# Kernel optimization log

Hardware: AMD Instinct MI355X
Metric: run time of the kernel (lower is better)

## Reference

```python
import jax, jax.numpy as jnp
import numpy as np

E = 16      # num_experts
K = 4       # num_experts_per_tok
H = 2048    # hidden_size
I = 1408    # moe_intermediate_size
SI = 5632   # shared expert intermediate size
CAP = 1024
NORM_TOPK = False


def setup_inputs() -> dict:
    key = jax.random.key(0)
    ks = jax.random.split(key, 9)
    def w(k, shape, fan_in):
        return jax.random.normal(k, shape, jnp.float32) * (fan_in ** -0.5)
    return {
        "hidden_states": jax.random.normal(ks[0], (1, 2048, H), jnp.float32),
        "gate_w":  w(ks[1], (E, H), H),        # router: Linear(H -> E), no bias
        "we_gate": w(ks[2], (E, I, H), H),     # per-expert gate_proj weights
        "we_up":   w(ks[3], (E, I, H), H),     # per-expert up_proj weights
        "we_down": w(ks[4], (E, H, I), I),     # per-expert down_proj weights
        "ws_gate": w(ks[5], (SI, H), H),       # shared expert gate_proj
        "ws_up":   w(ks[6], (SI, H), H),       # shared expert up_proj
        "ws_down": w(ks[7], (H, SI), SI),      # shared expert down_proj
        "sg_w":    w(ks[8], (1, H), H),        # shared_expert_gate: Linear(H -> 1)
    }


def reference(hidden_states, gate_w, we_gate, we_up, we_down,
              ws_gate, ws_up, ws_down, sg_w):
    B, S, Hd = hidden_states.shape
    x = hidden_states.reshape(-1, Hd)                      # [T, H]
    T = x.shape[0]

    # --- router ---
    router_logits = x @ gate_w.T                           # [T, E]
    probs = jax.nn.softmax(router_logits.astype(jnp.float32), axis=-1)
    topw, topi = jax.lax.top_k(probs, K)                   # [T, K]
    if NORM_TOPK:
        topw = topw / topw.sum(axis=-1, keepdims=True)

    # --- dispatch: flatten (token, slot) assignments ---
    A = T * K
    fe = topi.reshape(A)                                   # expert id per assignment
    fw = topw.reshape(A)                                   # routing weight per assignment
    ft = jnp.repeat(jnp.arange(T), K)                      # token id per assignment
    # position of each assignment within its expert (rank in arrival order)
    oh = jax.nn.one_hot(fe, E, dtype=jnp.int32)            # [A, E]
    pos = jnp.take_along_axis(jnp.cumsum(oh, axis=0) - 1, fe[:, None], axis=1)[:, 0]
    valid = pos < CAP
    # scatter tokens into per-expert buffers; overflow goes to dummy row CAP
    buf = jnp.zeros((E, CAP + 1, Hd), x.dtype)
    buf = buf.at[fe, jnp.where(valid, pos, CAP)].set(x[ft])[:, :CAP]  # [E, C, H]

    # --- per-expert SiLU-gated MLP (batched grouped GEMMs) ---
    g = jnp.einsum('ech,eih->eci', buf, we_gate)
    u = jnp.einsum('ech,eih->eci', buf, we_up)
    eo = jnp.einsum('eci,ehi->ech', jax.nn.silu(g) * u, we_down)      # [E, C, H]

    # --- combine: weighted scatter-add back to tokens ---
    ga = eo[fe, jnp.minimum(pos, CAP - 1)]                 # [A, H]
    wcomb = (fw * valid.astype(fw.dtype)).astype(x.dtype)
    y = jnp.zeros((T, Hd), x.dtype).at[ft].add(ga * wcomb[:, None])

    # --- shared expert with sigmoid gate ---
    sh = (jax.nn.silu(x @ ws_gate.T) * (x @ ws_up.T)) @ ws_down.T
    sh = jax.nn.sigmoid(x @ sg_w.T) * sh

    out = (y + sh).reshape(B, S, Hd)
    return out, router_logits
```

## Files before the change

### kernel.cpp

```cpp
#include <hip/hip_runtime.h>

#define T_TOK 2048
#define NE 16
#define KTOP 4
#define HD 2048
#define ID 1408
#define SID 5632
#define CAPACITY 1024

typedef __attribute__((ext_vector_type(8))) short short8;
typedef __attribute__((ext_vector_type(4))) float floatx4;

__device__ __forceinline__ short f2b(float f){
  union { float f; unsigned u; } v; v.f = f;
  unsigned r = v.u + 0x7fffu + ((v.u >> 16) & 1u);
  return (short)(r >> 16);
}
__device__ __forceinline__ float b2f(short s){
  union { float f; unsigned u; } v; v.u = ((unsigned)(unsigned short)s) << 16;
  return v.f;
}
__device__ __forceinline__ unsigned cvt_pk(float a, float b){
  unsigned r;
  asm("v_cvt_pk_bf16_f32 %0, %1, %2" : "=v"(r) : "v"(a), "v"(b));
  return r;
}
__device__ __forceinline__ short8 cvt8(float4 a, float4 b){
  union { unsigned d[4]; short8 s; } u;
  u.d[0] = cvt_pk(a.x, a.y); u.d[1] = cvt_pk(a.z, a.w);
  u.d[2] = cvt_pk(b.x, b.y); u.d[3] = cvt_pk(b.z, b.w);
  return u.s;
}
__device__ __forceinline__ void gl16(const void* g, void* l){
  __builtin_amdgcn_global_load_lds(
      (const __attribute__((address_space(1))) void*)g,
      (__attribute__((address_space(3))) void*)l, 16, 0, 0);
}

__global__ void moe_zero(int* __restrict__ counts){
  if (threadIdx.x < NE) counts[threadIdx.x] = 0;
}

__global__ void moe_router(const float* __restrict__ x,
                           const float* __restrict__ gate_w,
                           const float* __restrict__ sg_w,
                           float* __restrict__ logits_out,
                           short* __restrict__ xb,
                           int* __restrict__ counts,
                           int* __restrict__ slot_token,
                           float* __restrict__ slot_w,
                           int* __restrict__ tslot,
                           float* __restrict__ tw,
                           float* __restrict__ sg)
{
  int wave = threadIdx.x >> 6, lane = threadIdx.x & 63;
  int t = (blockIdx.x << 2) + wave;
  if (t >= T_TOK) return;
  const float4* xr = (const float4*)(x + (size_t)t * HD);
  short8* xbw = (short8*)(xb + (size_t)t * HD);
  float acc[17];
  #pragma unroll
  for (int e = 0; e < 17; ++e) acc[e] = 0.f;
  #pragma unroll
  for (int j = 0; j < 4; ++j){
    int i4 = (j * 64 + lane) * 2;
    float4 x0 = xr[i4], x1 = xr[i4 + 1];
    xbw[j * 64 + lane] = cvt8(x0, x1);
    #pragma unroll
    for (int e = 0; e < 16; ++e){
      const float4* gr = (const float4*)(gate_w + e * HD);
      float4 g0 = gr[i4], g1 = gr[i4 + 1];
      acc[e] += x0.x*g0.x + x0.y*g0.y + x0.z*g0.z + x0.w*g0.w
              + x1.x*g1.x + x1.y*g1.y + x1.z*g1.z + x1.w*g1.w;
    }
    const float4* sr = (const float4*)sg_w;
    float4 s0 = sr[i4], s1 = sr[i4 + 1];
    acc[16] += x0.x*s0.x + x0.y*s0.y + x0.z*s0.z + x0.w*s0.w
             + x1.x*s1.x + x1.y*s1.y + x1.z*s1.z + x1.w*s1.w;
  }
  #pragma unroll
  for (int e = 0; e < 17; ++e){
    float v = acc[e];
    #pragma unroll
    for (int off = 32; off > 0; off >>= 1) v += __shfl_xor(v, off, 64);
    acc[e] = v;
  }
  if (lane == 0){
    float m = acc[0];
    #pragma unroll
    for (int e = 1; e < 16; ++e) m = fmaxf(m, acc[e]);
    float p[16]; float s = 0.f;
    #pragma unroll
    for (int e = 0; e < 16; ++e){ p[e] = expf(acc[e] - m); s += p[e]; }
    float inv = 1.f / s;
    #pragma unroll
    for (int e = 0; e < 16; ++e) logits_out[t * 16 + e] = acc[e];
    unsigned used = 0;
    for (int k = 0; k < KTOP; ++k){
      float best = -1.f; int bi = 0;
      #pragma unroll
      for (int e = 0; e < 16; ++e){
        float pe = ((used >> e) & 1u) ? -1.f : p[e];
        if (pe > best){ best = pe; bi = e; }
      }
      used |= (1u << bi);
      int pos = atomicAdd(&counts[bi], 1);
      int enc = -1;
      if (pos < CAPACITY){
        slot_token[bi * CAPACITY + pos] = t;
        slot_w[bi * CAPACITY + pos] = best * inv;
        enc = bi * CAPACITY + pos;
      }
      tslot[t * KTOP + k] = enc;
      tw[t * KTOP + k] = best * inv;
    }
    sg[t] = 1.f / (1.f + expf(-acc[16]));
  }
}


__global__ __launch_bounds__(256) void moe_gateup(
    const short* __restrict__ Asrc,
    const float* __restrict__ Wg_, const float* __restrict__ Wu_,
    short* __restrict__ Out,
    const int* __restrict__ counts, const int* __restrict__ slot_token,
    int Ndim, int Kdim, int expert_mode, int mtiles, int ntiles)
{
  int nwg = gridDim.x;
  int wg = ((blockIdx.x & 7) * (nwg >> 3)) + (blockIdx.x >> 3);
  int m_t = wg % mtiles; wg /= mtiles;
  int n_t = wg % ntiles; int e = wg / ntiles;

  int cnt = T_TOK; size_t woff = 0; short* out = Out;
  if (expert_mode){
    cnt = counts[e]; if (cnt > CAPACITY) cnt = CAPACITY;
    if (m_t * 128 >= cnt) return;
    woff = (size_t)e * Ndim * Kdim;
    out = Out + (size_t)e * CAPACITY * Ndim;
  }
  const int m0 = m_t * 128, n0 = n_t * 64;

  __shared__ __align__(16) char smem[2][32768];

  const int tid = threadIdx.x;
  const int lane = tid & 63, wave = tid >> 6;
  const int wr = wave >> 1, wc = wave & 1;
  const int lrow = lane & 15, lk = lane >> 4;

  const int srow = tid >> 3, pslot = tid & 7;
  const int lslot = pslot ^ (srow & 7);

  const short* aptr[4];
  #pragma unroll
  for (int i = 0; i < 4; ++i){
    int p = m0 + i * 32 + srow;
    const short* base;
    if (expert_mode){
      int q = (p < cnt) ? p : 0;
      base = Asrc + (size_t)slot_token[e * CAPACITY + q] * Kdim;
    } else base = Asrc + (size_t)p * Kdim;
    aptr[i] = base + (lslot << 3);
  }
  const float *bsrc[4];
  #pragma unroll
  for (int i = 0; i < 2; ++i){
    size_t roff = (size_t)(n0 + i * 32 + srow) * Kdim + (lslot << 3);
    bsrc[i]     = Wg_ + woff + roff;
    bsrc[i + 2] = Wu_ + woff + roff;
  }

  const floatx4 vzero = {0.f, 0.f, 0.f, 0.f};
  floatx4 accg[4][2], accu[4][2];
  #pragma unroll
  for (int i = 0; i < 4; ++i)
    #pragma unroll
    for (int j = 0; j < 2; ++j){ accg[i][j] = vzero; accu[i][j] = vzero; }

  const int fxor = lrow & 7;
  const int arowb = (wr * 64 + lrow) << 7;
  const int browb = (wc * 32 + lrow) << 7;
  const int bwoff = 16384 + (tid << 4);

  float4 breg[4][2];
  #pragma unroll
  for (int i = 0; i < 4; ++i) gl16(aptr[i], smem[0] + i * 4096 + tid * 16);
  #pragma unroll
  for (int i = 0; i < 4; ++i){
    breg[i][0] = *(const float4*)(bsrc[i]);
    breg[i][1] = *(const float4*)(bsrc[i] + 4);
  }
  #pragma unroll
  for (int i = 0; i < 4; ++i)
    *(short8*)(smem[0] + bwoff + i * 4096) = cvt8(breg[i][0], breg[i][1]);
  __syncthreads();

  int cur = 0;
  for (int k0 = 0; k0 < Kdim; k0 += 64){
    const bool more = (k0 + 64) < Kdim;
    if (more){
      #pragma unroll
      for (int i = 0; i < 4; ++i) gl16(aptr[i] + k0 + 64, smem[cur ^ 1] + i * 4096 + tid * 16);
      #pragma unroll
      for (int i = 0; i < 4; ++i){
        breg[i][0] = *(const float4*)(bsrc[i] + k0 + 64);
        breg[i][1] = *(const float4*)(bsrc[i] + k0 + 68);
      }
    }
    const char* bb = smem[cur];
    #pragma unroll
    for (int kh = 0; kh < 2; ++kh){
      const int soff = (((kh << 2) | lk) ^ fxor) << 4;
      short8 a[4], bg[2], bu[2];
      #pragma unroll
      for (int mf = 0; mf < 4; ++mf)
        a[mf] = *(const short8*)(bb + arowb + (mf << 11) + soff);
      #pragma unroll
      for (int nf = 0; nf < 2; ++nf){
        bg[nf] = *(const short8*)(bb + 16384 + browb + (nf << 11) + soff);
        bu[nf] = *(const short8*)(bb + 24576 + browb + (nf << 11) + soff);
      }
      #pragma unroll
      for (int mf = 0; mf < 4; ++mf)
        #pragma unroll
        for (int nf = 0; nf < 2; ++nf){
          accg[mf][nf] = __builtin_amdgcn_mfma_f32_16x16x32_bf16(a[mf], bg[nf], accg[mf][nf], 0, 0, 0);
          accu[mf][nf] = __builtin_amdgcn_mfma_f32_16x16x32_bf16(a[mf], bu[nf], accu[mf][nf], 0, 0, 0);
        }
    }
    if (more){
      #pragma unroll
      for (int i = 0; i < 4; ++i)
        *(short8*)(smem[cur ^ 1] + bwoff + i * 4096) = cvt8(breg[i][0], breg[i][1]);
    }
    __syncthreads();
    cur ^= 1;
  }

  const int colbase = n0 + wc * 32 + lrow;
  #pragma unroll
  for (int mf = 0; mf < 4; ++mf){
    int pr = m0 + wr * 64 + mf * 16 + lk * 4;
    #pragma unroll
    for (int nf = 0; nf < 2; ++nf){
      floatx4 g4 = accg[mf][nf], u4 = accu[mf][nf];
      int col = colbase + nf * 16;
      #pragma unroll
      for (int r = 0; r < 4; ++r){
        float gv = g4[r], uv = u4[r];
        float a = (gv / (1.f + __expf(-gv))) * uv;
        out[(size_t)(pr + r) * Ndim + col] = f2b(a);
      }
    }
  }
}

template<int NF>
__global__ __launch_bounds__(256) void moe_down(
    const short* __restrict__ Asrc, const float* __restrict__ Wd_,
    float* __restrict__ y, short* __restrict__ eo,
    const int* __restrict__ counts, const int* __restrict__ slot_token,
    const float* __restrict__ slot_w, const float* __restrict__ sgate,
    int Kdim, int expert_mode, int mtiles, int ntiles)
{
  constexpr int BN = NF * 32;
  int nwg = gridDim.x;
  int wg = ((blockIdx.x & 7) * (nwg >> 3)) + (blockIdx.x >> 3);
  int m_t = wg % mtiles; wg /= mtiles;
  int n_t = wg % ntiles; int e = wg / ntiles;

  int cnt = T_TOK; const short* ab = Asrc; size_t woff = 0;
  if (expert_mode){
    cnt = counts[e]; if (cnt > CAPACITY) cnt = CAPACITY;
    if (m_t * 128 >= cnt) return;
    ab = Asrc + (size_t)e * CAPACITY * Kdim;
    woff = (size_t)e * HD * Kdim;
  }
  const int m0 = m_t * 128, n0 = n_t * BN;

  __shared__ __align__(16) char smem[2][16384 + NF * 4096];

  const int tid = threadIdx.x;
  const int lane = tid & 63, wave = tid >> 6;
  const int wr = wave >> 1, wc = wave & 1;
  const int lrow = lane & 15, lk = lane >> 4;

  const int srow = tid >> 3, pslot = tid & 7;
  const int lslot = pslot ^ (srow & 7);

  const short* aptr[4];
  #pragma unroll
  for (int i = 0; i < 4; ++i)
    aptr[i] = ab + (size_t)(m0 + i * 32 + srow) * Kdim + (lslot << 3);
  const float* bsrc[NF];
  #pragma unroll
  for (int i = 0; i < NF; ++i)
    bsrc[i] = Wd_ + woff + (size_t)(n0 + i * 32 + srow) * Kdim + (lslot << 3);

  const floatx4 vzero = {0.f, 0.f, 0.f, 0.f};
  floatx4 acc[4][NF];
  #pragma unroll
  for (int i = 0; i < 4; ++i)
    #pragma unroll
    for (int j = 0; j < NF; ++j) acc[i][j] = vzero;

  const int fxor = lrow & 7;
  const int arowb = (wr * 64 + lrow) << 7;
  const int browb = (wc * (NF * 16) + lrow) << 7;
  const int bwoff = 16384 + (tid << 4);

  float4 breg[NF][2];
  #pragma unroll
  for (int i = 0; i < 4; ++i) gl16(aptr[i], smem[0] + i * 4096 + tid * 16);
  #pragma unroll
  for (int i = 0; i < NF; ++i){
    breg[i][0] = *(const float4*)(bsrc[i]);
    breg[i][1] = *(const float4*)(bsrc[i] + 4);
  }
  #pragma unroll
  for (int i = 0; i < NF; ++i)
    *(short8*)(smem[0] + bwoff + i * 4096) = cvt8(breg[i][0], breg[i][1]);
  __syncthreads();

  int cur = 0;
  for (int k0 = 0; k0 < Kdim; k0 += 64){
    const bool more = (k0 + 64) < Kdim;
    if (more){
      #pragma unroll
      for (int i = 0; i < 4; ++i) gl16(aptr[i] + k0 + 64, smem[cur ^ 1] + i * 4096 + tid * 16);
      #pragma unroll
      for (int i = 0; i < NF; ++i){
        breg[i][0] = *(const float4*)(bsrc[i] + k0 + 64);
        breg[i][1] = *(const float4*)(bsrc[i] + k0 + 68);
      }
    }
    const char* bb = smem[cur];
    #pragma unroll
    for (int kh = 0; kh < 2; ++kh){
      const int soff = (((kh << 2) | lk) ^ fxor) << 4;
      short8 a[4], b[NF];
      #pragma unroll
      for (int mf = 0; mf < 4; ++mf)
        a[mf] = *(const short8*)(bb + arowb + (mf << 11) + soff);
      #pragma unroll
      for (int nf = 0; nf < NF; ++nf)
        b[nf] = *(const short8*)(bb + 16384 + browb + (nf << 11) + soff);
      #pragma unroll
      for (int mf = 0; mf < 4; ++mf)
        #pragma unroll
        for (int nf = 0; nf < NF; ++nf)
          acc[mf][nf] = __builtin_amdgcn_mfma_f32_16x16x32_bf16(a[mf], b[nf], acc[mf][nf], 0, 0, 0);
    }
    if (more){
      #pragma unroll
      for (int i = 0; i < NF; ++i)
        *(short8*)(smem[cur ^ 1] + bwoff + i * 4096) = cvt8(breg[i][0], breg[i][1]);
    }
    __syncthreads();
    cur ^= 1;
  }

  const int colb = n0 + wc * (NF * 16) + lrow;
  if (expert_mode){
    if (eo){
      #pragma unroll
      for (int mf = 0; mf < 4; ++mf){
        int pr = m0 + wr * 64 + mf * 16 + lk * 4;
        #pragma unroll
        for (int r = 0; r < 4; ++r){
          int p = pr + r;
          #pragma unroll
          for (int nf = 0; nf < NF; ++nf)
            eo[(size_t)(e * CAPACITY + p) * HD + colb + nf * 16] = f2b(acc[mf][nf][r]);
        }
      }
    } else {
      #pragma unroll
      for (int mf = 0; mf < 4; ++mf){
        int pr = m0 + wr * 64 + mf * 16 + lk * 4;
        #pragma unroll
        for (int r = 0; r < 4; ++r){
          int p = pr + r;
          if (p < cnt){
            int tok = slot_token[e * CAPACITY + p];
            float w = slot_w[e * CAPACITY + p];
            #pragma unroll
            for (int nf = 0; nf < NF; ++nf)
              atomicAdd(&y[(size_t)tok * HD + colb + nf * 16], w * acc[mf][nf][r]);
          }
        }
      }
    }
  } else {
    #pragma unroll
    for (int mf = 0; mf < 4; ++mf){
      int pr = m0 + wr * 64 + mf * 16 + lk * 4;
      #pragma unroll
      for (int r = 0; r < 4; ++r){
        int t = pr + r;
        float sv = sgate[t];
        #pragma unroll
        for (int nf = 0; nf < NF; ++nf)
          y[(size_t)t * HD + colb + nf * 16] = sv * acc[mf][nf][r];
      }
    }
  }
}

__global__ void moe_combine(const short* __restrict__ eo,
                            const int* __restrict__ tslot,
                            const float* __restrict__ tw,
                            float* __restrict__ y)
{
  int t = blockIdx.x;
  int o = threadIdx.x << 3;
  float* yp = y + (size_t)t * HD + o;
  float4 a0 = *(const float4*)yp, a1 = *(const float4*)(yp + 4);
  float acc[8] = {a0.x, a0.y, a0.z, a0.w, a1.x, a1.y, a1.z, a1.w};
  #pragma unroll
  for (int k = 0; k < KTOP; ++k){
    int s = tslot[t * KTOP + k];
    if (s >= 0){
      float w = tw[t * KTOP + k];
      short8 v = *(const short8*)(eo + (size_t)s * HD + o);
      #pragma unroll
      for (int j = 0; j < 8; ++j) acc[j] += w * b2f(v[j]);
    }
  }
  float4 r0 = {acc[0], acc[1], acc[2], acc[3]};
  float4 r1 = {acc[4], acc[5], acc[6], acc[7]};
  *(float4*)yp = r0; *(float4*)(yp + 4) = r1;
}

extern "C" void kernel_launch(void* const* d_in, const int* in_sizes, int n_in,
                              void* d_out, int out_size, void* d_ws, size_t ws_size,
                              hipStream_t stream)
{
  (void)in_sizes; (void)n_in; (void)out_size;
  const float* x       = (const float*)d_in[0];
  const float* gate_w  = (const float*)d_in[1];
  const float* we_gate = (const float*)d_in[2];
  const float* we_up   = (const float*)d_in[3];
  const float* we_down = (const float*)d_in[4];
  const float* wsg     = (const float*)d_in[5];
  const float* wsu     = (const float*)d_in[6];
  const float* wsd     = (const float*)d_in[7];
  const float* sg_w    = (const float*)d_in[8];

  float* y      = (float*)d_out;
  float* logits = y + (size_t)T_TOK * HD;

  const size_t SZ_XB  = (size_t)T_TOK * HD * 2;
  const size_t SZ_ACT = (size_t)NE * CAPACITY * ID * 2;
  const size_t SZ_ACS = (size_t)T_TOK * SID * 2;
  const size_t SZ_EO  = (size_t)NE * CAPACITY * HD * 2;
  const size_t SZ_SMALL = 65536 + 65536 + 32768 + 32768 + 256 + 8192;

  const size_t NEED_B = SZ_XB + SZ_ACT + SZ_ACS + SZ_SMALL;
  const size_t NEED_A = NEED_B + SZ_EO;

  char* ws = (char*)d_ws;
  size_t off = 0;
  short* xb   = (short*)(ws + off); off += SZ_XB;
  short* act  = (short*)(ws + off); off += SZ_ACT;
  short* acts = (short*)(ws + off); off += SZ_ACS;
  short* eo   = (short*)(ws + off);
  if (ws_size >= NEED_A) off += SZ_EO; else eo = nullptr;
  int*   slot_token = (int*)  (ws + off); off += 65536;
  float* slot_w     = (float*)(ws + off); off += 65536;
  int*   tslot      = (int*)  (ws + off); off += 32768;
  float* tw         = (float*)(ws + off); off += 32768;
  int*   counts     = (int*)  (ws + off); off += 256;
  float* sg         = (float*)(ws + off);

  moe_zero<<<1, 64, 0, stream>>>(counts);
  moe_router<<<512, 256, 0, stream>>>(x, gate_w, sg_w, logits, xb,
                                      counts, slot_token, slot_w, tslot, tw, sg);
  moe_gateup<<<16 * 88, 256, 0, stream>>>(xb, wsg, wsu, acts,
                                          nullptr, nullptr, SID, HD, 0, 16, 88);
  moe_gateup<<<8 * 22 * NE, 256, 0, stream>>>(xb, we_gate, we_up, act,
                                              counts, slot_token, ID, HD, 1, 8, 22);
  moe_down<2><<<16 * 32, 256, 0, stream>>>(acts, wsd, y, nullptr, nullptr, nullptr,
                                           nullptr, sg, SID, 0, 16, 32);
  moe_down<4><<<8 * 16 * NE, 256, 0, stream>>>(act, we_down, y, eo, counts, slot_token,
                                               slot_w, nullptr, ID, 1, 8, 16);
  if (eo) moe_combine<<<T_TOK, 256, 0, stream>>>(eo, tslot, tw, y);
}
```

Measured before the change: 800.4 us.

## Pre-convert weights to bf16 and stream GEMM tiles via direct-to-LDS loads

Adds a conversion kernel that casts all expert and shared-expert fp32 weights to bf16 in workspace on every call. The gate/up and down GEMMs then load both operands with global_load_lds, using a smaller 32-wide K step and explicit waitcnt/barrier double buffering. This removes the register round trip and per-tile fp32->bf16 conversion in the GEMM loops, and halves weight bytes on the repeated per-M-tile reads. In exchange it adds a full read of the fp32 weights plus a bf16 write each call, and a much larger workspace. It also drops the workspace size check and reuses the converted gate-weight buffer as the eo scratch.

```diff
diff --git a/kernel.cpp b/kernel.cpp
--- a/kernel.cpp
+++ b/kernel.cpp
@@ -39,6 +39,29 @@
 
 __global__ void moe_zero(int* __restrict__ counts){
   if (threadIdx.x < NE) counts[threadIdx.x] = 0;
+}
+
+__global__ void moe_convert(const float* __restrict__ eg, const float* __restrict__ eu,
+                            const float* __restrict__ ed, const float* __restrict__ sgp,
+                            const float* __restrict__ sup, const float* __restrict__ sdp,
+                            short* __restrict__ dst)
+{
+  const long long R8 = 1441792LL;
+  const int r = blockIdx.y;
+  const float* src;
+  if      (r <  4) src = eg  + (long long)r       * R8 * 8;
+  else if (r <  8) src = eu  + (long long)(r - 4) * R8 * 8;
+  else if (r < 12) src = ed  + (long long)(r - 8) * R8 * 8;
+  else if (r == 12) src = sgp;
+  else if (r == 13) src = sup;
+  else              src = sdp;
+  short8* d = (short8*)dst + (long long)r * R8;
+  const long long stride = (long long)gridDim.x * blockDim.x;
+  for (long long i = (long long)blockIdx.x * blockDim.x + threadIdx.x; i < R8; i += stride){
+    float4 f0 = ((const float4*)src)[i * 2];
+    float4 f1 = ((const float4*)src)[i * 2 + 1];
+    d[i] = cvt8(f0, f1);
+  }
 }
 
 __global__ void moe_router(const float* __restrict__ x,
@@ -119,9 +142,21 @@
 }
 
 
+#define GEMM_PREAMBLE \
+  const int tid = threadIdx.x; \
+  const int lane = tid & 63, wave = tid >> 6; \
+  const int wr = wave >> 1, wc = wave & 1; \
+  const int lrow = lane & 15, lk = lane >> 4; \
+  const int s_th = (tid & 7) ^ ((tid >> 3) & 7); \
+  const int koff = (s_th & 3) << 3; \
+  const int rloc = ((tid >> 3) << 1) + (s_th >> 2); \
+  const int lb = lrow >> 1; \
+  const int soff = (((((lrow & 1) << 2) | lk) ^ (lb & 7)) << 4); \
+  const int abase = (wr * 32 + lb) * 128 + soff;
+
 __global__ __launch_bounds__(256) void moe_gateup(
     const short* __restrict__ Asrc,
-    const float* __restrict__ Wg_, const float* __restrict__ Wu_,
+    const short* __restrict__ Wg, const short* __restrict__ Wu,
     short* __restrict__ Out,
     const int* __restrict__ counts, const int* __restrict__ slot_token,
     int Ndim, int Kdim, int expert_mode, int mtiles, int ntiles)
@@ -140,34 +175,24 @@
   }
   const int m0 = m_t * 128, n0 = n_t * 64;
 
-  __shared__ __align__(16) char smem[2][32768];
-
-  const int tid = threadIdx.x;
-  const int lane = tid & 63, wave = tid >> 6;
-  const int wr = wave >> 1, wc = wave & 1;
-  const int lrow = lane & 15, lk = lane >> 4;
-
-  const int srow = tid >> 3, pslot = tid & 7;
-  const int lslot = pslot ^ (srow & 7);
-
-  const short* aptr[4];
-  #pragma unroll
-  for (int i = 0; i < 4; ++i){
-    int p = m0 + i * 32 + srow;
+  __shared__ __align__(16) char smem[2][16384];
+
+  GEMM_PREAMBLE
+  const int gbase = 8192 + (wc * 16 + lb) * 128 + soff;
+
+  const short* aP[2];
+  #pragma unroll
+  for (int i = 0; i < 2; ++i){
+    int p = m0 + i * 64 + rloc;
     const short* base;
     if (expert_mode){
       int q = (p < cnt) ? p : 0;
       base = Asrc + (size_t)slot_token[e * CAPACITY + q] * Kdim;
     } else base = Asrc + (size_t)p * Kdim;
-    aptr[i] = base + (lslot << 3);
-  }
-  const float *bsrc[4];
-  #pragma unroll
-  for (int i = 0; i < 2; ++i){
-    size_t roff = (size_t)(n0 + i * 32 + srow) * Kdim + (lslot << 3);
-    bsrc[i]     = Wg_ + woff + roff;
-    bsrc[i + 2] = Wu_ + woff + roff;
-  }
+    aP[i] = base + koff;
+  }
+  const short* bgP = Wg + woff + (size_t)(n0 + rloc) * Kdim + koff;
+  const short* buP = Wu + woff + (size_t)(n0 + rloc) * Kdim + koff;
 
   const floatx4 vzero = {0.f, 0.f, 0.f, 0.f};
   floatx4 accg[4][2], accu[4][2];
@@ -176,65 +201,41 @@
     #pragma unroll
     for (int j = 0; j < 2; ++j){ accg[i][j] = vzero; accu[i][j] = vzero; }
 
-  const int fxor = lrow & 7;
-  const int arowb = (wr * 64 + lrow) << 7;
-  const int browb = (wc * 32 + lrow) << 7;
-  const int bwoff = 16384 + (tid << 4);
-
-  float4 breg[4][2];
-  #pragma unroll
-  for (int i = 0; i < 4; ++i) gl16(aptr[i], smem[0] + i * 4096 + tid * 16);
-  #pragma unroll
-  for (int i = 0; i < 4; ++i){
-    breg[i][0] = *(const float4*)(bsrc[i]);
-    breg[i][1] = *(const float4*)(bsrc[i] + 4);
-  }
-  #pragma unroll
-  for (int i = 0; i < 4; ++i)
-    *(short8*)(smem[0] + bwoff + i * 4096) = cvt8(breg[i][0], breg[i][1]);
-  __syncthreads();
-
+#define GU_STAGE(B, K) { char* _b = smem[B]; \
+    gl16(aP[0] + (K), _b + tid * 16); \
+    gl16(aP[1] + (K), _b + 4096 + tid * 16); \
+    gl16(bgP + (K),   _b + 8192 + tid * 16); \
+    gl16(buP + (K),   _b + 12288 + tid * 16); }
+
+#define GU_COMPUTE(B) { const char* bb = smem[B]; \
+    short8 a[4], bg[2], bu[2]; \
+    _Pragma("unroll") \
+    for (int mf = 0; mf < 4; ++mf) a[mf] = *(const short8*)(bb + abase + mf * 1024); \
+    _Pragma("unroll") \
+    for (int nf = 0; nf < 2; ++nf){ \
+      bg[nf] = *(const short8*)(bb + gbase + nf * 1024); \
+      bu[nf] = *(const short8*)(bb + gbase + 4096 + nf * 1024); } \
+    _Pragma("unroll") \
+    for (int mf = 0; mf < 4; ++mf) \
+      _Pragma("unroll") \
+      for (int nf = 0; nf < 2; ++nf){ \
+        accg[mf][nf] = __builtin_amdgcn_mfma_f32_16x16x32_bf16(a[mf], bg[nf], accg[mf][nf], 0, 0, 0); \
+        accu[mf][nf] = __builtin_amdgcn_mfma_f32_16x16x32_bf16(a[mf], bu[nf], accu[mf][nf], 0, 0, 0); } }
+
+  const int NSTEP = Kdim >> 5;
+  GU_STAGE(0, 0)
   int cur = 0;
-  for (int k0 = 0; k0 < Kdim; k0 += 64){
-    const bool more = (k0 + 64) < Kdim;
-    if (more){
-      #pragma unroll
-      for (int i = 0; i < 4; ++i) gl16(aptr[i] + k0 + 64, smem[cur ^ 1] + i * 4096 + tid * 16);
-      #pragma unroll
-      for (int i = 0; i < 4; ++i){
-        breg[i][0] = *(const float4*)(bsrc[i] + k0 + 64);
-        breg[i][1] = *(const float4*)(bsrc[i] + k0 + 68);
-      }
-    }
-    const char* bb = smem[cur];
-    #pragma unroll
-    for (int kh = 0; kh < 2; ++kh){
-      const int soff = (((kh << 2) | lk) ^ fxor) << 4;
-      short8 a[4], bg[2], bu[2];
-      #pragma unroll
-      for (int mf = 0; mf < 4; ++mf)
-        a[mf] = *(const short8*)(bb + arowb + (mf << 11) + soff);
-      #pragma unroll
-      for (int nf = 0; nf < 2; ++nf){
-        bg[nf] = *(const short8*)(bb + 16384 + browb + (nf << 11) + soff);
-        bu[nf] = *(const short8*)(bb + 24576 + browb + (nf << 11) + soff);
-      }
-      #pragma unroll
-      for (int mf = 0; mf < 4; ++mf)
-        #pragma unroll
-        for (int nf = 0; nf < 2; ++nf){
-          accg[mf][nf] = __builtin_amdgcn_mfma_f32_16x16x32_bf16(a[mf], bg[nf], accg[mf][nf], 0, 0, 0);
-          accu[mf][nf] = __builtin_amdgcn_mfma_f32_16x16x32_bf16(a[mf], bu[nf], accu[mf][nf], 0, 0, 0);
-        }
-    }
-    if (more){
-      #pragma unroll
-      for (int i = 0; i < 4; ++i)
-        *(short8*)(smem[cur ^ 1] + bwoff + i * 4096) = cvt8(breg[i][0], breg[i][1]);
-    }
-    __syncthreads();
+  for (int s = 0; s < NSTEP - 1; ++s){
+    GU_STAGE(cur ^ 1, (s + 1) << 5)
+    asm volatile("s_waitcnt vmcnt(4)" ::: "memory");
+    asm volatile("s_barrier" ::: "memory");
+    GU_COMPUTE(cur)
+    asm volatile("s_barrier" ::: "memory");
     cur ^= 1;
   }
+  asm volatile("s_waitcnt vmcnt(0)" ::: "memory");
+  asm volatile("s_barrier" ::: "memory");
+  GU_COMPUTE(cur)
 
   const int colbase = n0 + wc * 32 + lrow;
   #pragma unroll
@@ -256,13 +257,12 @@
 
 template<int NF>
 __global__ __launch_bounds__(256) void moe_down(
-    const short* __restrict__ Asrc, const float* __restrict__ Wd_,
+    const short* __restrict__ Asrc, const short* __restrict__ Wd,
     float* __restrict__ y, short* __restrict__ eo,
     const int* __restrict__ counts, const int* __restrict__ slot_token,
     const float* __restrict__ slot_w, const float* __restrict__ sgate,
     int Kdim, int expert_mode, int mtiles, int ntiles)
 {
-  constexpr int BN = NF * 32;
   int nwg = gridDim.x;
   int wg = ((blockIdx.x & 7) * (nwg >> 3)) + (blockIdx.x >> 3);
   int m_t = wg % mtiles; wg /= mtiles;
@@ -275,26 +275,21 @@
     ab = Asrc + (size_t)e * CAPACITY * Kdim;
     woff = (size_t)e * HD * Kdim;
   }
-  const int m0 = m_t * 128, n0 = n_t * BN;
-
-  __shared__ __align__(16) char smem[2][16384 + NF * 4096];
-
-  const int tid = threadIdx.x;
-  const int lane = tid & 63, wave = tid >> 6;
-  const int wr = wave >> 1, wc = wave & 1;
-  const int lrow = lane & 15, lk = lane >> 4;
-
-  const int srow = tid >> 3, pslot = tid & 7;
-  const int lslot = pslot ^ (srow & 7);
-
-  const short* aptr[4];
-  #pragma unroll
-  for (int i = 0; i < 4; ++i)
-    aptr[i] = ab + (size_t)(m0 + i * 32 + srow) * Kdim + (lslot << 3);
-  const float* bsrc[NF];
-  #pragma unroll
-  for (int i = 0; i < NF; ++i)
-    bsrc[i] = Wd_ + woff + (size_t)(n0 + i * 32 + srow) * Kdim + (lslot << 3);
+  const int m0 = m_t * 128, n0 = n_t * (NF * 32);
+
+  __shared__ __align__(16) char smem[2][8192 + NF * 2048];
+
+  GEMM_PREAMBLE
+  const int bbase = 8192 + (wc * (NF * 8) + lb) * 128 + soff;
+
+  const short* aP[2];
+  #pragma unroll
+  for (int i = 0; i < 2; ++i)
+    aP[i] = ab + (size_t)(m0 + i * 64 + rloc) * Kdim + koff;
+  const short* bP[NF / 2];
+  #pragma unroll
+  for (int i = 0; i < NF / 2; ++i)
+    bP[i] = Wd + woff + (size_t)(n0 + i * 64 + rloc) * Kdim + koff;
 
   const floatx4 vzero = {0.f, 0.f, 0.f, 0.f};
   floatx4 acc[4][NF];
@@ -303,61 +298,40 @@
     #pragma unroll
     for (int j = 0; j < NF; ++j) acc[i][j] = vzero;
 
-  const int fxor = lrow & 7;
-  const int arowb = (wr * 64 + lrow) << 7;
-  const int browb = (wc * (NF * 16) + lrow) << 7;
-  const int bwoff = 16384 + (tid << 4);
-
-  float4 breg[NF][2];
-  #pragma unroll
-  for (int i = 0; i < 4; ++i) gl16(aptr[i], smem[0] + i * 4096 + tid * 16);
-  #pragma unroll
-  for (int i = 0; i < NF; ++i){
-    breg[i][0] = *(const float4*)(bsrc[i]);
-    breg[i][1] = *(const float4*)(bsrc[i] + 4);
-  }
-  #pragma unroll
-  for (int i = 0; i < NF; ++i)
-    *(short8*)(smem[0] + bwoff + i * 4096) = cvt8(breg[i][0], breg[i][1]);
-  __syncthreads();
-
+#define DN_STAGE(B, K) { char* _b = smem[B]; \
+    gl16(aP[0] + (K), _b + tid * 16); \
+    gl16(aP[1] + (K), _b + 4096 + tid * 16); \
+    _Pragma("unroll") \
+    for (int i = 0; i < NF / 2; ++i) \
+      gl16(bP[i] + (K), _b + 8192 + i * 4096 + tid * 16); }
+
+#define DN_COMPUTE(B) { const char* bb = smem[B]; \
+    short8 a[4], b[NF]; \
+    _Pragma("unroll") \
+    for (int mf = 0; mf < 4; ++mf) a[mf] = *(const short8*)(bb + abase + mf * 1024); \
+    _Pragma("unroll") \
+    for (int nf = 0; nf < NF; ++nf) b[nf] = *(const short8*)(bb + bbase + nf * 1024); \
+    _Pragma("unroll") \
+    for (int mf = 0; mf < 4; ++mf) \
+      _Pragma("unroll") \
+      for (int nf = 0; nf < NF; ++nf) \
+        acc[mf][nf] = __builtin_amdgcn_mfma_f32_16x16x32_bf16(a[mf], b[nf], acc[mf][nf], 0, 0, 0); }
+
+  const int NSTEP = Kdim >> 5;
+  DN_STAGE(0, 0)
   int cur = 0;
-  for (int k0 = 0; k0 < Kdim; k0 += 64){
-    const bool more = (k0 + 64) < Kdim;
-    if (more){
-      #pragma unroll
-      for (int i = 0; i < 4; ++i) gl16(aptr[i] + k0 + 64, smem[cur ^ 1] + i * 4096 + tid * 16);
-      #pragma unroll
-      for (int i = 0; i < NF; ++i){
-        breg[i][0] = *(const float4*)(bsrc[i] + k0 + 64);
-        breg[i][1] = *(const float4*)(bsrc[i] + k0 + 68);
-      }
-    }
-    const char* bb = smem[cur];
-    #pragma unroll
-    for (int kh = 0; kh < 2; ++kh){
-      const int soff = (((kh << 2) | lk) ^ fxor) << 4;
-      short8 a[4], b[NF];
-      #pragma unroll
-      for (int mf = 0; mf < 4; ++mf)
-        a[mf] = *(const short8*)(bb + arowb + (mf << 11) + soff);
-      #pragma unroll
-      for (int nf = 0; nf < NF; ++nf)
-        b[nf] = *(const short8*)(bb + 16384 + browb + (nf << 11) + soff);
-      #pragma unroll
-      for (int mf = 0; mf < 4; ++mf)
-        #pragma unroll
-        for (int nf = 0; nf < NF; ++nf)
-          acc[mf][nf] = __builtin_amdgcn_mfma_f32_16x16x32_bf16(a[mf], b[nf], acc[mf][nf], 0, 0, 0);
-    }
-    if (more){
-      #pragma unroll
-      for (int i = 0; i < NF; ++i)
-        *(short8*)(smem[cur ^ 1] + bwoff + i * 4096) = cvt8(breg[i][0], breg[i][1]);
-    }
-    __syncthreads();
+  for (int s = 0; s < NSTEP - 1; ++s){
+    DN_STAGE(cur ^ 1, (s + 1) << 5)
+    if (NF == 4) asm volatile("s_waitcnt vmcnt(4)" ::: "memory");
+    else         asm volatile("s_waitcnt vmcnt(3)" ::: "memory");
+    asm volatile("s_barrier" ::: "memory");
+    DN_COMPUTE(cur)
+    asm volatile("s_barrier" ::: "memory");
     cur ^= 1;
   }
+  asm volatile("s_waitcnt vmcnt(0)" ::: "memory");
+  asm volatile("s_barrier" ::: "memory");
+  DN_COMPUTE(cur)
 
   const int colb = n0 + wc * (NF * 16) + lrow;
   if (expert_mode){
@@ -435,7 +409,7 @@
                               void* d_out, int out_size, void* d_ws, size_t ws_size,
                               hipStream_t stream)
 {
-  (void)in_sizes; (void)n_in; (void)out_size;
+  (void)in_sizes; (void)n_in; (void)out_size; (void)ws_size;
   const float* x       = (const float*)d_in[0];
   const float* gate_w  = (const float*)d_in[1];
   const float* we_gate = (const float*)d_in[2];
@@ -449,22 +423,15 @@
   float* y      = (float*)d_out;
   float* logits = y + (size_t)T_TOK * HD;
 
-  const size_t SZ_XB  = (size_t)T_TOK * HD * 2;
-  const size_t SZ_ACT = (size_t)NE * CAPACITY * ID * 2;
-  const size_t SZ_ACS = (size_t)T_TOK * SID * 2;
-  const size_t SZ_EO  = (size_t)NE * CAPACITY * HD * 2;
-  const size_t SZ_SMALL = 65536 + 65536 + 32768 + 32768 + 256 + 8192;
-
-  const size_t NEED_B = SZ_XB + SZ_ACT + SZ_ACS + SZ_SMALL;
-  const size_t NEED_A = NEED_B + SZ_EO;
+  const size_t N_EW = (size_t)NE * ID * HD;
+  const size_t N_SW = (size_t)SID * HD;
 
   char* ws = (char*)d_ws;
   size_t off = 0;
-  short* xb   = (short*)(ws + off); off += SZ_XB;
-  short* act  = (short*)(ws + off); off += SZ_ACT;
-  short* acts = (short*)(ws + off); off += SZ_ACS;
-  short* eo   = (short*)(ws + off);
-  if (ws_size >= NEED_A) off += SZ_EO; else eo = nullptr;
+  short* xb   = (short*)(ws + off); off += (size_t)T_TOK * HD * 2;
+  short* wb   = (short*)(ws + off); off += (3 * N_EW + 3 * N_SW) * 2;
+  short* act  = (short*)(ws + off); off += (size_t)NE * CAPACITY * ID * 2;
+  short* acts = (short*)(ws + off); off += (size_t)T_TOK * SID * 2;
   int*   slot_token = (int*)  (ws + off); off += 65536;
   float* slot_w     = (float*)(ws + off); off += 65536;
   int*   tslot      = (int*)  (ws + off); off += 32768;
@@ -472,16 +439,26 @@
   int*   counts     = (int*)  (ws + off); off += 256;
   float* sg         = (float*)(ws + off);
 
+  short* wbeg = wb;
+  short* wbeu = wb + N_EW;
+  short* wbed = wb + 2 * N_EW;
+  short* wbsg = wb + 3 * N_EW;
+  short* wbsu = wb + 3 * N_EW + N_SW;
+  short* wbsd = wb + 3 * N_EW + 2 * N_SW;
+  short* eo = wbeg;
+
   moe_zero<<<1, 64, 0, stream>>>(counts);
+  moe_convert<<<dim3(256, 15), 256, 0, stream>>>(we_gate, we_up, we_down,
+                                                 wsg, wsu, wsd, wb);
   moe_router<<<512, 256, 0, stream>>>(x, gate_w, sg_w, logits, xb,
                                       counts, slot_token, slot_w, tslot, tw, sg);
-  moe_gateup<<<16 * 88, 256, 0, stream>>>(xb, wsg, wsu, acts,
+  moe_gateup<<<16 * 88, 256, 0, stream>>>(xb, wbsg, wbsu, acts,
                                           nullptr, nullptr, SID, HD, 0, 16, 88);
-  moe_gateup<<<8 * 22 * NE, 256, 0, stream>>>(xb, we_gate, we_up, act,
+  moe_gateup<<<8 * 22 * NE, 256, 0, stream>>>(xb, wbeg, wbeu, act,
                                               counts, slot_token, ID, HD, 1, 8, 22);
-  moe_down<2><<<16 * 32, 256, 0, stream>>>(acts, wsd, y, nullptr, nullptr, nullptr,
+  moe_down<2><<<16 * 32, 256, 0, stream>>>(acts, wbsd, y, nullptr, nullptr, nullptr,
                                            nullptr, sg, SID, 0, 16, 32);
-  moe_down<4><<<8 * 16 * NE, 256, 0, stream>>>(act, we_down, y, eo, counts, slot_token,
+  moe_down<4><<<8 * 16 * NE, 256, 0, stream>>>(act, wbed, y, eo, counts, slot_token,
                                                slot_w, nullptr, ID, 1, 8, 16);
-  if (eo) moe_combine<<<T_TOK, 256, 0, stream>>>(eo, tslot, tw, y);
-}
+  moe_combine<<<T_TOK, 256, 0, stream>>>(eo, tslot, tw, y);
+}
```

Measured after the change: 860.7 us. +7.5%, slower.
